# Kernel tuning notes

Hardware: AMD Instinct MI355X
Metric: run time of the kernel (lower is better)

Reference implementation:

```python
import jax, jax.numpy as jnp
import numpy as np

K = 16          # k_neighbours
BIG = 1e9       # distance penalty for masked senders


def setup_inputs() -> dict:
    key = jax.random.key(0)
    ks = jax.random.split(key, 8)
    B, N, F, H, FO = 64, 512, 64, 128, 64
    nodes = jax.random.normal(ks[0], (B, N, F), jnp.float32)
    mask = jax.random.randint(ks[1], (B, N), 0, 2, jnp.int32)

    def w(k_, sh):
        return jax.random.normal(k_, sh, jnp.float32) * (1.0 / np.sqrt(sh[0]).astype(np.float32))

    We1 = w(ks[2], (2 * F, H)); be1 = jnp.zeros((H,), jnp.float32)
    We2 = w(ks[3], (H, H));     be2 = jnp.zeros((H,), jnp.float32)
    Wn1 = w(ks[4], (F + H, H)); bn1 = jnp.zeros((H,), jnp.float32)
    Wn2 = w(ks[5], (H, FO));    bn2 = jnp.zeros((FO,), jnp.float32)
    return dict(nodes=nodes, mask=mask, We1=We1, be1=be1, We2=We2, be2=be2,
                Wn1=Wn1, bn1=bn1, Wn2=Wn2, bn2=bn2)


def reference(nodes, mask, We1, be1, We2, be2, Wn1, bn1, Wn2, bn2):
    # nodes: [B,N,F] ; mask: [B,N] (1 = real node, 0 = padding)
    m = mask.astype(nodes.dtype)                      # [B,N]
    x = nodes * m[..., None]                          # zero padded nodes

    # --- dynamic kNN graph (euclidean_squared + top_k, no self connection) ---
    sq = jnp.sum(x * x, axis=-1)                      # [B,N]
    dist = jnp.abs(sq[:, :, None] + sq[:, None, :]
                   - 2.0 * jnp.einsum('bnf,bmf->bnm', x, x))  # [B,N,N]
    dist = dist + BIG * (1.0 - m)[:, None, :]         # never select masked senders
    _, idx = jax.lax.top_k(-dist, K + 1)              # [B,N,K+1]
    idx = idx[..., 1:]                                # drop self connection -> [B,N,K]

    # --- gather sender features / masks along edges ---
    gathered = jax.vmap(lambda xf, ib: xf[ib])(x, idx)    # [B,N,K,F]
    smask = jax.vmap(lambda mv, ib: mv[ib])(m, idx)       # [B,N,K]
    recv = jnp.broadcast_to(x[:, :, None, :], gathered.shape)
    edges = jnp.concatenate([recv, gathered], axis=-1)    # [B,N,K,2F] ('concat' aggregation)

    # --- edge MLP (gather-compute) ---
    h = jax.nn.relu(edges @ We1 + be1)
    h = jax.nn.relu(h @ We2 + be2)                        # [B,N,K,H]

    # --- masked mean pooling over edges (scatter back to nodes) ---
    emask = m[:, :, None] * smask                         # edge valid iff both endpoints valid
    h = h * emask[..., None]
    cnt = jnp.maximum(jnp.sum(emask, axis=-1, keepdims=True), 1.0)  # [B,N,1]
    pooled = jnp.sum(h, axis=2) / cnt                     # [B,N,H]

    # --- node update MLP ---
    nh = jnp.concatenate([x, pooled], axis=-1)            # [B,N,F+H]
    out = jax.nn.relu(nh @ Wn1 + bn1) @ Wn2 + bn2         # [B,N,FO]
    return out * m[..., None]                             # zero padded nodes in output
```

## Files before the change

### kernel.cpp

```cpp
#include <hip/hip_runtime.h>

#define DI __device__ __forceinline__

typedef __bf16 bf16_t;
typedef __bf16 bf16x4 __attribute__((ext_vector_type(4)));
typedef __bf16 bf16x8 __attribute__((ext_vector_type(8)));
typedef float f32x4 __attribute__((ext_vector_type(4)));
typedef unsigned long long u64;


DI bf16_t f2b(float f) {
  unsigned u = __float_as_uint(f);
  unsigned r = (u + 0x7fffu + ((u >> 16) & 1u)) >> 16;
  return __builtin_bit_cast(bf16_t, (unsigned short)r);
}
DI float b2f(bf16_t h) {
  return __uint_as_float(((unsigned)__builtin_bit_cast(unsigned short, h)) << 16);
}
DI f32x4 zero4() { f32x4 z = {0.f, 0.f, 0.f, 0.f}; return z; }

DI bf16x8 make_frag(const float* p, bool wantlo) {
  float4 v0 = *(const float4*)p;
  float4 v1 = *(const float4*)(p + 4);
  float vv[8] = {v0.x, v0.y, v0.z, v0.w, v1.x, v1.y, v1.z, v1.w};
  bf16x8 a;
#pragma unroll
  for (int j = 0; j < 8; ++j) {
    bf16_t hi = f2b(vv[j]);
    a[j] = wantlo ? f2b(vv[j] - b2f(hi)) : hi;
  }
  return a;
}

DI u64 u64min(u64 a, u64 b) { return a < b ? a : b; }
template <int CTRL>
DI u64 dpp_u64(u64 v) {
  int lo = (int)(unsigned)(v & 0xffffffffull);
  int hi = (int)(unsigned)(v >> 32);
  int tlo = __builtin_amdgcn_update_dpp(0, lo, CTRL, 0xF, 0xF, true);
  int thi = __builtin_amdgcn_update_dpp(0, hi, CTRL, 0xF, 0xF, true);
  return (((u64)(unsigned)thi) << 32) | (unsigned)tlo;
}
template <int CTRL>
DI float dpp_f32(float v) {
  int t = __builtin_amdgcn_update_dpp(0, (int)__float_as_uint(v), CTRL, 0xF, 0xF, true);
  return __uint_as_float((unsigned)t);
}
DI u64 rowmin_u64(u64 v) {
  v = u64min(v, dpp_u64<0xB1>(v));
  v = u64min(v, dpp_u64<0x4E>(v));
  v = u64min(v, dpp_u64<0x141>(v));
  v = u64min(v, dpp_u64<0x140>(v));
  return v;
}
DI float rowsum_f32(float v) {
  v += dpp_f32<0xB1>(v);
  v += dpp_f32<0x4E>(v);
  v += dpp_f32<0x141>(v);
  v += dpp_f32<0x140>(v);
  return v;
}
DI void bitonic16(u64* a) {
#pragma unroll
  for (int k = 2; k <= 16; k <<= 1)
#pragma unroll
    for (int j = k >> 1; j > 0; j >>= 1)
#pragma unroll
      for (int i = 0; i < 16; ++i) {
        const int l = i ^ j;
        if (l > i) {
          const bool up = ((i & k) == 0);
          const bool sw = up ? (a[i] > a[l]) : (a[i] < a[l]);
          const u64 t0 = a[i], t1 = a[l];
          a[i] = sw ? t1 : t0;
          a[l] = sw ? t0 : t1;
        }
      }
}

__global__ void __launch_bounds__(256) kfuse(const float* __restrict__ nodes,
    const int* __restrict__ mask,
    const float* __restrict__ We1, const float* __restrict__ We2,
    const float* __restrict__ Wn1, const float* __restrict__ Wn2,
    float* __restrict__ x, bf16_t* __restrict__ xhi, bf16_t* __restrict__ xlo,
    float* __restrict__ sq, int* __restrict__ vlist, int* __restrict__ vcnt,
    bf16_t* __restrict__ W1p, bf16_t* __restrict__ W2p,
    bf16_t* __restrict__ Wn1p, bf16_t* __restrict__ Wn2p) {
  const int blk = blockIdx.x, t = threadIdx.x;
  __shared__ int cnts[8];
  __shared__ int basep[8];

  if (blk < 512) {
    const int b = blk >> 3, n0 = (blk & 7) * 64;
#pragma unroll
    for (int i = 0; i < 4; ++i) {
      const int idx = t + 256 * i;
      const int gi = b * 512 + n0 + (idx >> 4);
      const int fo = (idx & 15) * 4;
      const float fm = (float)mask[gi];
      const size_t ro = (size_t)gi * 64;
      float4 v = *(const float4*)(nodes + ro + fo);
      v.x *= fm; v.y *= fm; v.z *= fm; v.w *= fm;
      *(float4*)(x + ro + fo) = v;
      float vv[4] = {v.x, v.y, v.z, v.w};
      bf16x4 hh, ll;
#pragma unroll
      for (int k = 0; k < 4; ++k) {
        bf16_t hi = f2b(vv[k]);
        hh[k] = hi;
        ll[k] = f2b(vv[k] - b2f(hi));
      }
      *(bf16x4*)(xhi + ro + fo) = hh;
      *(bf16x4*)(xlo + ro + fo) = ll;
      float s = v.x * v.x + v.y * v.y + v.z * v.z + v.w * v.w;
      s = rowsum_f32(s);
      if ((t & 15) == 0) sq[gi] = s;
    }
  } else if (blk < 576) {
    const int b = blk - 512, lane = t & 63, w = t >> 6;
    unsigned long long bal[2]; int flag[2];
#pragma unroll
    for (int h = 0; h < 2; ++h) {
      flag[h] = (mask[b * 512 + h * 256 + t] != 0);
      bal[h] = __ballot(flag[h]);
      if (lane == 0) cnts[h * 4 + w] = __popcll(bal[h]);
    }
    __syncthreads();
    if (t == 0) {
      int a = 0;
      for (int c = 0; c < 8; ++c) { basep[c] = a; a += cnts[c]; }
      vcnt[b] = a;
    }
    __syncthreads();
#pragma unroll
    for (int h = 0; h < 2; ++h) {
      if (flag[h]) {
        const unsigned long long lt = (lane == 0) ? 0ull : (~0ull >> (64 - lane));
        const int pos = basep[h * 4 + w] + __popcll(bal[h] & lt);
        vlist[b * 512 + pos] = h * 256 + t;
      }
    }
  } else {
    int p = (blk - 576) * 256 + t;
    const float* W; bf16_t* dst; int K, Nn, local, mode;
    if (p < 4096)       { W = We1; dst = W1p;  K = 128; Nn = 128; mode = 0; local = p; }
    else if (p < 8192)  { W = We2; dst = W2p;  K = 128; Nn = 128; mode = 1; local = p - 4096; }
    else if (p < 14336) { W = Wn1; dst = Wn1p; K = 192; Nn = 128; mode = 0; local = p - 8192; }
    else                { W = Wn2; dst = Wn2p; K = 128; Nn = 64;  mode = 1; local = p - 14336; }
    int lane = local & 63;
    int nnt = (Nn >> 4);
    int chunk = local >> 6;
    int nt = chunk % nnt;
    int s = chunk / nnt;
    int n = nt * 16 + (lane & 15);
    int kbase = s * 32 + ((lane >> 4) * 8);
    bf16x8 v;
#pragma unroll
    for (int j = 0; j < 8; ++j) {
      int kp = kbase + j;
      int region = kp / K;
      int kk = kp - region * K;
      float w = W[kk * Nn + n];
      bf16_t hi = f2b(w);
      v[j] = (mode == 1 && region == 1) ? f2b(w - b2f(hi)) : hi;
    }
    *(bf16x8*)(dst + (size_t)local * 8) = v;
  }
}

__global__ void __launch_bounds__(256) kknn(const float* __restrict__ x,
    const float* __restrict__ sq, const int* __restrict__ vlist,
    const int* __restrict__ vcnt, int* __restrict__ idxg) {
  const int b = blockIdx.x & 63, tile = blockIdx.x >> 6;
  const int nv = vcnt[b];
  if (tile * 16 >= nv) return;
  const int t = threadIdx.x, lane = t & 63, w = t >> 6;
  const int i = lane >> 4, d = lane & 15;
  __shared__ float sqs[512];
  __shared__ int vls[512];
  __shared__ __align__(16) float xr[16 * 64];
  __shared__ __align__(16) float xc[64 * 68];
  for (int k = t; k < 512; k += 256) { sqs[k] = sq[b * 512 + k]; vls[k] = vlist[b * 512 + k]; }
  __syncthreads();
  const float* xb = x + (size_t)b * 512 * 64;
  {
    const int r = t >> 4, f4 = (t & 15) * 4;
    const int slot = tile * 16 + r;
    const int row = vls[slot < nv ? slot : 0];
    *(float4*)(xr + r * 64 + f4) = *(const float4*)(xb + (size_t)row * 64 + f4);
  }
  const int rslot = tile * 16 + w * 4 + i;
  const bool vrow = (rslot < nv);
  const int nrow = vls[rslot < nv ? rslot : 0];
  const float sqn = sqs[nrow];
  __syncthreads();
  const float4 xn = *(const float4*)(xr + (w * 4 + i) * 64 + d * 4);

  float dotv[32];
#pragma unroll
  for (int j = 0; j < 32; ++j) dotv[j] = 0.f;

#pragma unroll
  for (int cb = 0; cb < 8; ++cb) {
    if (cb * 64 < nv) {
      __syncthreads();
      {
        const int fo = (t & 15) * 4;
#pragma unroll
        for (int p = 0; p < 4; ++p) {
          const int cl = (t >> 4) + p * 16;
          const int c = cb * 64 + cl;
          if (c < nv)
            *(float4*)(xc + cl * 68 + fo) = *(const float4*)(xb + (size_t)vls[c] * 64 + fo);
        }
      }
      __syncthreads();
#pragma unroll
      for (int q = 0; q < 4; ++q) {
        float dq = 0.f;
#pragma unroll 4
        for (int cc = 0; cc < 16; ++cc) {
          const float4 xm = *(const float4*)(xc + (q * 16 + cc) * 68 + d * 4);
          float p = xn.x * xm.x;
          p = fmaf(xn.y, xm.y, p);
          p = fmaf(xn.z, xm.z, p);
          p = fmaf(xn.w, xm.w, p);
          p = rowsum_f32(p);
          dq = (d == cc) ? p : dq;
        }
        dotv[cb * 4 + q] = dq;
      }
    }
  }

  const u64 INF64 = ~0ull;
  u64 s1[16], s2[16];
#pragma unroll
  for (int j = 0; j < 16; ++j) { s1[j] = INF64; s2[j] = INF64; }
#pragma unroll
  for (int j = 0; j < 32; ++j) {
    if (j * 16 < nv) {
      const int c = j * 16 + d;
      const int m = vls[c < nv ? c : 0];
      const float dd = fabsf(sqn + sqs[m] - 2.f * dotv[j]);
      const u64 key = (((u64)__float_as_uint(dd)) << 32) | (unsigned)m;
      const bool ok = (c < nv) && (m != nrow);
      if (j < 16) s1[j] = ok ? key : INF64;
      else        s2[j - 16] = ok ? key : INF64;
    }
  }
  bitonic16(s1);
  const bool two = (nv > 256);
  if (two) bitonic16(s2);

  int res = nrow;
#pragma unroll
  for (int ts = 0; ts < 16; ++ts) {
    const u64 head = two ? u64min(s1[0], s2[0]) : s1[0];
    const u64 wmin = rowmin_u64(head);
    if (d == ts) res = (wmin == INF64) ? nrow : (int)(unsigned)(wmin & 0xffffffffull);
    const bool w1 = (wmin != INF64) && (s1[0] == wmin);
#pragma unroll
    for (int k = 0; k < 15; ++k) s1[k] = w1 ? s1[k + 1] : s1[k];
    s1[15] = w1 ? INF64 : s1[15];
    if (two) {
      const bool w2 = (wmin != INF64) && (s2[0] == wmin);
#pragma unroll
      for (int k = 0; k < 15; ++k) s2[k] = w2 ? s2[k + 1] : s2[k];
      s2[15] = w2 ? INF64 : s2[15];
    }
  }
  if (vrow) idxg[((size_t)b * 512 + rslot) * 16 + d] = res;
}

__global__ void __launch_bounds__(256, 2) kedge(const bf16_t* __restrict__ xhi,
    const bf16_t* __restrict__ xlo, const int* __restrict__ idxg,
    const int* __restrict__ vlist, const int* __restrict__ vcnt,
    const bf16_t* __restrict__ W1p, const bf16_t* __restrict__ W2p,
    const float* __restrict__ be1, const float* __restrict__ be2,
    float* __restrict__ pooled) {
  __shared__ __align__(16) bf16_t wbuf[32768];
  __shared__ __align__(16) bf16_t hfrag[4][2][1024];
  const int t = threadIdx.x, lane = t & 63, w = t >> 6;
  const int q = lane >> 4, e = lane & 15;
  const int bb = blockIdx.x & 63;
  const int s0 = ((blockIdx.x >> 6) * 4 + w) * 2;

  {
    const uint4* s1 = (const uint4*)W1p;
    const uint4* s2 = (const uint4*)W2p;
    uint4* dst = (uint4*)wbuf;
#pragma unroll
    for (int i = 0; i < 8; ++i) dst[t + 256 * i] = s1[t + 256 * i];
#pragma unroll
    for (int i = 0; i < 8; ++i) dst[2048 + t + 256 * i] = s2[t + 256 * i];
  }
  __syncthreads();

  const int nv = vcnt[bb];
  if (s0 >= nv) return;

  int vl[2], sv[2];
  {
#pragma unroll
    for (int u = 0; u < 2; ++u) {
      const int sl = (s0 + u) < nv ? (s0 + u) : 0;
      vl[u] = vlist[bb * 512 + sl];
      sv[u] = idxg[((size_t)(bb * 512 + sl) << 4) + e];
    }
  }

  for (int base = s0; base < nv; base += 64) {
    const bool act1 = (base + 1) < nv;
    const int gid0 = bb * 512 + vl[0];
    const int gid1 = bb * 512 + vl[1];
    const size_t rb0 = (size_t)gid0 << 6;
    const size_t rb1 = (size_t)gid1 << 6;
    const size_t nb0 = (size_t)(bb * 512 + sv[0]) << 6;
    const size_t nb1 = (size_t)(bb * 512 + sv[1]) << 6;

    bf16x8 af[2][8];
#pragma unroll
    for (int k = 0; k < 4; ++k) {
      const int off = (k & 1) * 32 + q * 8;
      const bf16_t* pl = (k >> 1) ? xlo : xhi;
      af[0][k]     = *(const bf16x8*)(pl + rb0 + off);
      af[1][k]     = *(const bf16x8*)(pl + rb1 + off);
      af[0][4 + k] = *(const bf16x8*)(pl + nb0 + off);
      af[1][4 + k] = *(const bf16x8*)(pl + nb1 + off);
    }

    int nvl[2] = {vl[0], vl[1]}, nsv[2] = {sv[0], sv[1]};
    {
      const int nb = base + 64;
      if (nb < nv) {
#pragma unroll
        for (int u = 0; u < 2; ++u) {
          const int sl = (nb + u) < nv ? (nb + u) : 0;
          nvl[u] = vlist[bb * 512 + sl];
          nsv[u] = idxg[((size_t)(bb * 512 + sl) << 4) + e];
        }
      }
    }

    f32x4 acc[2][8];
#pragma unroll
    for (int u = 0; u < 2; ++u)
#pragma unroll
      for (int nt = 0; nt < 8; ++nt) acc[u][nt] = zero4();

#pragma unroll
    for (int ph = 0; ph < 2; ++ph)
#pragma unroll
      for (int k = 0; k < 4; ++k) {
        const bf16_t* wb = wbuf + (ph * 2 + (k & 1)) * 4096;
        const bf16x8 a0 = af[0][ph * 4 + k];
        const bf16x8 a1 = af[1][ph * 4 + k];
#pragma unroll
        for (int nt = 0; nt < 8; ++nt) {
          const bf16x8 bfv = *(const bf16x8*)(wb + (nt * 64 + lane) * 8);
          acc[0][nt] = __builtin_amdgcn_mfma_f32_16x16x32_bf16(a0, bfv, acc[0][nt], 0, 0, 0);
          acc[1][nt] = __builtin_amdgcn_mfma_f32_16x16x32_bf16(a1, bfv, acc[1][nt], 0, 0, 0);
        }
      }

    f32x4 acc2[2][8];
#pragma unroll
    for (int u = 0; u < 2; ++u)
#pragma unroll
      for (int nt = 0; nt < 8; ++nt) acc2[u][nt] = zero4();

#pragma unroll
    for (int hh = 0; hh < 2; ++hh) {
#pragma unroll
      for (int u = 0; u < 2; ++u)
#pragma unroll
        for (int nt4 = 0; nt4 < 4; ++nt4) {
          const int nt = hh * 4 + nt4;
          const int cc = nt * 16 + e;
          const float bv = be1[cc];
          const int bse = (((cc >> 5) & 1) * 64 + q * 4 + 16 * ((cc >> 3) & 3)) * 8 + (cc & 7);
#pragma unroll
          for (int r = 0; r < 4; ++r)
            hfrag[w][u][bse + r * 8] = f2b(fmaxf(acc[u][nt][r] + bv, 0.f));
        }
#pragma unroll
      for (int sl = 0; sl < 2; ++sl) {
        const int f = hh * 2 + sl;
        const bf16x8 a20 = *(const bf16x8*)(&hfrag[w][0][(sl * 64 + lane) * 8]);
        const bf16x8 a21 = *(const bf16x8*)(&hfrag[w][1][(sl * 64 + lane) * 8]);
        const bf16_t* wb2 = wbuf + 16384 + f * 4096;
#pragma unroll
        for (int nt = 0; nt < 8; ++nt) {
          const bf16x8 bfv = *(const bf16x8*)(wb2 + (nt * 64 + lane) * 8);
          acc2[0][nt] = __builtin_amdgcn_mfma_f32_16x16x32_bf16(a20, bfv, acc2[0][nt], 0, 0, 0);
          acc2[1][nt] = __builtin_amdgcn_mfma_f32_16x16x32_bf16(a21, bfv, acc2[1][nt], 0, 0, 0);
        }
      }
    }

#pragma unroll
    for (int u = 0; u < 2; ++u) {
      if (u == 0 || act1) {
        const int gid = u ? gid1 : gid0;
#pragma unroll
        for (int nt = 0; nt < 8; ++nt) {
          const float bv = be2[nt * 16 + e];
          float part = 0.f;
#pragma unroll
          for (int r = 0; r < 4; ++r) part += fmaxf(acc2[u][nt][r] + bv, 0.f);
          part += __shfl_xor(part, 16, 64);
          part += __shfl_xor(part, 32, 64);
          if (lane < 16) pooled[(size_t)gid * 128 + nt * 16 + lane] = part * 0.0625f;
        }
      }
    }

    vl[0] = nvl[0]; vl[1] = nvl[1];
    sv[0] = nsv[0]; sv[1] = nsv[1];
  }
}

__global__ void __launch_bounds__(256) knode(const float* __restrict__ x,
    const float* __restrict__ pooled, const int* __restrict__ mask,
    const bf16_t* __restrict__ Wn1p, const bf16_t* __restrict__ Wn2p,
    const float* __restrict__ bn1, const float* __restrict__ bn2,
    float* __restrict__ out) {
  __shared__ __align__(16) bf16_t wbuf[8192];
  __shared__ __align__(16) bf16_t hfrag[4][2][2048];
  const int t = threadIdx.x, lane = t & 63, w = t >> 6;
  const int q = lane >> 4, e = lane & 15;
  int nodebase[2];
#pragma unroll
  for (int u = 0; u < 2; ++u) nodebase[u] = (blockIdx.x * 8 + w * 2 + u) * 16;

  f32x4 acc[2][8];
#pragma unroll
  for (int u = 0; u < 2; ++u)
#pragma unroll
    for (int nt = 0; nt < 8; ++nt) acc[u][nt] = zero4();

#pragma unroll
  for (int ph = 0; ph < 3; ++ph) {
    __syncthreads();
    {
      const uint4* src = (const uint4*)(Wn1p + (size_t)ph * 8192);
      uint4* dst = (uint4*)wbuf;
#pragma unroll
      for (int i = 0; i < 4; ++i) dst[t + 256 * i] = src[t + 256 * i];
    }
    __syncthreads();
#pragma unroll
    for (int k = 0; k < 4; ++k) {
      const int s = 2 * ph + (k & 1) + (k >> 1) * 6;
      const bool wantlo = (s >= 6);
      const int sr = wantlo ? (s - 6) : s;
      const int col = sr * 32 + q * 8;
      bf16x8 af[2];
#pragma unroll
      for (int u = 0; u < 2; ++u) {
        const int node = nodebase[u] + e;
        const float* p = (col < 64) ? (x + (size_t)node * 64 + col)
                                    : (pooled + (size_t)node * 128 + (col - 64));
        af[u] = make_frag(p, wantlo);
      }
      const int bslab = s & 1;
#pragma unroll
      for (int nt = 0; nt < 8; ++nt) {
        const bf16x8 bfv = *(const bf16x8*)(wbuf + bslab * 4096 + (nt * 64 + lane) * 8);
#pragma unroll
        for (int u = 0; u < 2; ++u)
          acc[u][nt] = __builtin_amdgcn_mfma_f32_16x16x32_bf16(af[u], bfv, acc[u][nt], 0, 0, 0);
      }
    }
  }

#pragma unroll
  for (int u = 0; u < 2; ++u) {
#pragma unroll
    for (int nt = 0; nt < 8; ++nt) {
      const int cc = nt * 16 + e;
      const float bv = bn1[cc];
      const int base = ((cc >> 5) * 64 + (q * 4) + 16 * ((cc >> 3) & 3)) * 8 + (cc & 7);
#pragma unroll
      for (int r = 0; r < 4; ++r) {
        float h = fmaxf(acc[u][nt][r] + bv, 0.f);
        hfrag[w][u][base + r * 8] = f2b(h);
      }
    }
  }

  f32x4 acc2[2][4];
#pragma unroll
  for (int u = 0; u < 2; ++u)
#pragma unroll
    for (int nt = 0; nt < 4; ++nt) acc2[u][nt] = zero4();

  __syncthreads();
  {
    const uint4* src = (const uint4*)Wn2p;
    uint4* dst = (uint4*)wbuf;
#pragma unroll
    for (int i = 0; i < 4; ++i) dst[t + 256 * i] = src[t + 256 * i];
  }
  __syncthreads();
#pragma unroll
  for (int sl = 0; sl < 4; ++sl) {
    bf16x8 af[2];
#pragma unroll
    for (int u = 0; u < 2; ++u)
      af[u] = *(const bf16x8*)(&hfrag[w][u][(sl * 64 + lane) * 8]);
#pragma unroll
    for (int nt = 0; nt < 4; ++nt) {
      const bf16x8 bfv = *(const bf16x8*)(wbuf + sl * 2048 + (nt * 64 + lane) * 8);
#pragma unroll
      for (int u = 0; u < 2; ++u)
        acc2[u][nt] = __builtin_amdgcn_mfma_f32_16x16x32_bf16(af[u], bfv, acc2[u][nt], 0, 0, 0);
    }
  }

#pragma unroll
  for (int u = 0; u < 2; ++u) {
    int mm[4];
#pragma unroll
    for (int r = 0; r < 4; ++r) mm[r] = mask[nodebase[u] + q * 4 + r];
#pragma unroll
    for (int nt = 0; nt < 4; ++nt) {
      const float bv = bn2[nt * 16 + e];
#pragma unroll
      for (int r = 0; r < 4; ++r) {
        const int node = nodebase[u] + q * 4 + r;
        out[(size_t)node * 64 + nt * 16 + e] = (acc2[u][nt][r] + bv) * (float)mm[r];
      }
    }
  }
}

extern "C" void kernel_launch(void* const* d_in, const int* in_sizes, int n_in,
                              void* d_out, int out_size, void* d_ws, size_t ws_size,
                              hipStream_t stream) {
  const float* nodes = (const float*)d_in[0];
  const int*   mask  = (const int*)d_in[1];
  const float* We1   = (const float*)d_in[2];
  const float* be1   = (const float*)d_in[3];
  const float* We2   = (const float*)d_in[4];
  const float* be2   = (const float*)d_in[5];
  const float* Wn1   = (const float*)d_in[6];
  const float* bn1   = (const float*)d_in[7];
  const float* Wn2   = (const float*)d_in[8];
  const float* bn2   = (const float*)d_in[9];
  float* out = (float*)d_out;

  char* p = (char*)d_ws;
  auto alloc = [&](size_t bytes) -> char* {
    char* r = p;
    p += (bytes + 255) & ~(size_t)255;
    return r;
  };
  float*  x      = (float*)alloc((size_t)32768 * 64 * 4);
  bf16_t* xhi    = (bf16_t*)alloc((size_t)32768 * 64 * 2);
  bf16_t* xlo    = (bf16_t*)alloc((size_t)32768 * 64 * 2);
  float*  sq     = (float*)alloc((size_t)32768 * 4);
  int*    vlist  = (int*)alloc((size_t)32768 * 4);
  int*    vcnt   = (int*)alloc((size_t)64 * 4);
  int*    idxg   = (int*)alloc((size_t)32768 * 16 * 4);
  float*  pooled = (float*)alloc((size_t)32768 * 128 * 4);
  bf16_t* W1p    = (bf16_t*)alloc((size_t)8 * 8 * 64 * 8 * 2);
  bf16_t* W2p    = (bf16_t*)alloc((size_t)8 * 8 * 64 * 8 * 2);
  bf16_t* Wn1p   = (bf16_t*)alloc((size_t)12 * 8 * 64 * 8 * 2);
  bf16_t* Wn2p   = (bf16_t*)alloc((size_t)8 * 4 * 64 * 8 * 2);
  if ((size_t)(p - (char*)d_ws) > ws_size) return;

  kfuse<<<640, 256, 0, stream>>>(nodes, mask, We1, We2, Wn1, Wn2,
                                 x, xhi, xlo, sq, vlist, vcnt, W1p, W2p, Wn1p, Wn2p);
  kknn<<<2048, 256, 0, stream>>>(x, sq, vlist, vcnt, idxg);
  kedge<<<512, 256, 0, stream>>>(xhi, xlo, idxg, vlist, vcnt, W1p, W2p, be1, be2, pooled);
  knode<<<256, 256, 0, stream>>>(x, pooled, mask, Wn1p, Wn2p, bn1, bn2, out);
}
```

Before: 189.2 us.

## Compute kNN dot products with split-bf16 MFMA instead of scalar FP32 shuffles

Replaces the FP32 per-lane dot-product loop with cross-lane row reductions in the kNN kernel by 16x16x32 bf16 MFMA tiles. The hi and lo bf16 parts are combined with four MFMAs per K-chunk to approximate FP32 accuracy. Candidate rows are loaded straight from global memory into registers, with the next tile prefetched, instead of being staged through shared memory. The dot matrix is written to shared memory for the top-k stage. This is meant to remove the shuffle-heavy ALU work and the repeated syncthreads, at the cost of a small precision change that could alter near-tie neighbour choices.

```diff
diff --git a/kernel.cpp b/kernel.cpp
--- a/kernel.cpp
+++ b/kernel.cpp
@@ -168,7 +168,8 @@
   }
 }
 
-__global__ void __launch_bounds__(256) kknn(const float* __restrict__ x,
+__global__ void __launch_bounds__(256) kknn(const bf16_t* __restrict__ xhi,
+    const bf16_t* __restrict__ xlo,
     const float* __restrict__ sq, const int* __restrict__ vlist,
     const int* __restrict__ vcnt, int* __restrict__ idxg) {
   const int b = blockIdx.x & 63, tile = blockIdx.x >> 6;
@@ -178,60 +179,69 @@
   const int i = lane >> 4, d = lane & 15;
   __shared__ float sqs[512];
   __shared__ int vls[512];
-  __shared__ __align__(16) float xr[16 * 64];
-  __shared__ __align__(16) float xc[64 * 68];
+  __shared__ __align__(16) float S[16 * 520];
   for (int k = t; k < 512; k += 256) { sqs[k] = sq[b * 512 + k]; vls[k] = vlist[b * 512 + k]; }
   __syncthreads();
-  const float* xb = x + (size_t)b * 512 * 64;
-  {
-    const int r = t >> 4, f4 = (t & 15) * 4;
-    const int slot = tile * 16 + r;
-    const int row = vls[slot < nv ? slot : 0];
-    *(float4*)(xr + r * 64 + f4) = *(const float4*)(xb + (size_t)row * 64 + f4);
-  }
+
+  const size_t xb = (size_t)b * 512 * 64;
+
+  const int aslot = tile * 16 + d;
+  const int arow = vls[aslot < nv ? aslot : 0];
+  bf16x8 ah[2], al[2];
+#pragma unroll
+  for (int kh = 0; kh < 2; ++kh) {
+    ah[kh] = *(const bf16x8*)(xhi + xb + (size_t)arow * 64 + kh * 32 + i * 8);
+    al[kh] = *(const bf16x8*)(xlo + xb + (size_t)arow * 64 + kh * 32 + i * 8);
+  }
+
   const int rslot = tile * 16 + w * 4 + i;
   const bool vrow = (rslot < nv);
   const int nrow = vls[rslot < nv ? rslot : 0];
   const float sqn = sqs[nrow];
+
+  int crs[8];
+#pragma unroll
+  for (int jj = 0; jj < 8; ++jj) {
+    const int c = (w + 4 * jj) * 16 + d;
+    crs[jj] = vls[c < nv ? c : 0];
+  }
+
+  bf16x8 bh[2], bl[2];
+  if (w * 16 < nv) {
+#pragma unroll
+    for (int kh = 0; kh < 2; ++kh) {
+      bh[kh] = *(const bf16x8*)(xhi + xb + (size_t)crs[0] * 64 + kh * 32 + i * 8);
+      bl[kh] = *(const bf16x8*)(xlo + xb + (size_t)crs[0] * 64 + kh * 32 + i * 8);
+    }
+  }
+  for (int jj = 0; jj < 8; ++jj) {
+    const int ct = w + 4 * jj;
+    if (ct * 16 >= nv) break;
+    bf16x8 nbh[2], nbl[2];
+    const bool pre = (jj < 7) && ((w + 4 * (jj + 1)) * 16 < nv);
+    if (pre) {
+#pragma unroll
+      for (int kh = 0; kh < 2; ++kh) {
+        nbh[kh] = *(const bf16x8*)(xhi + xb + (size_t)crs[jj + 1] * 64 + kh * 32 + i * 8);
+        nbl[kh] = *(const bf16x8*)(xlo + xb + (size_t)crs[jj + 1] * 64 + kh * 32 + i * 8);
+      }
+    }
+    f32x4 acc = zero4();
+#pragma unroll
+    for (int kh = 0; kh < 2; ++kh) {
+      acc = __builtin_amdgcn_mfma_f32_16x16x32_bf16(ah[kh], bh[kh], acc, 0, 0, 0);
+      acc = __builtin_amdgcn_mfma_f32_16x16x32_bf16(ah[kh], bl[kh], acc, 0, 0, 0);
+      acc = __builtin_amdgcn_mfma_f32_16x16x32_bf16(al[kh], bh[kh], acc, 0, 0, 0);
+      acc = __builtin_amdgcn_mfma_f32_16x16x32_bf16(al[kh], bl[kh], acc, 0, 0, 0);
+    }
+#pragma unroll
+    for (int r = 0; r < 4; ++r) S[(i * 4 + r) * 520 + ct * 16 + d] = acc[r];
+    if (pre) {
+#pragma unroll
+      for (int kh = 0; kh < 2; ++kh) { bh[kh] = nbh[kh]; bl[kh] = nbl[kh]; }
+    }
+  }
   __syncthreads();
-  const float4 xn = *(const float4*)(xr + (w * 4 + i) * 64 + d * 4);
-
-  float dotv[32];
-#pragma unroll
-  for (int j = 0; j < 32; ++j) dotv[j] = 0.f;
-
-#pragma unroll
-  for (int cb = 0; cb < 8; ++cb) {
-    if (cb * 64 < nv) {
-      __syncthreads();
-      {
-        const int fo = (t & 15) * 4;
-#pragma unroll
-        for (int p = 0; p < 4; ++p) {
-          const int cl = (t >> 4) + p * 16;
-          const int c = cb * 64 + cl;
-          if (c < nv)
-            *(float4*)(xc + cl * 68 + fo) = *(const float4*)(xb + (size_t)vls[c] * 64 + fo);
-        }
-      }
-      __syncthreads();
-#pragma unroll
-      for (int q = 0; q < 4; ++q) {
-        float dq = 0.f;
-#pragma unroll 4
-        for (int cc = 0; cc < 16; ++cc) {
-          const float4 xm = *(const float4*)(xc + (q * 16 + cc) * 68 + d * 4);
-          float p = xn.x * xm.x;
-          p = fmaf(xn.y, xm.y, p);
-          p = fmaf(xn.z, xm.z, p);
-          p = fmaf(xn.w, xm.w, p);
-          p = rowsum_f32(p);
-          dq = (d == cc) ? p : dq;
-        }
-        dotv[cb * 4 + q] = dq;
-      }
-    }
-  }
 
   const u64 INF64 = ~0ull;
   u64 s1[16], s2[16];
@@ -242,7 +252,8 @@
     if (j * 16 < nv) {
       const int c = j * 16 + d;
       const int m = vls[c < nv ? c : 0];
-      const float dd = fabsf(sqn + sqs[m] - 2.f * dotv[j]);
+      const float dot = S[(w * 4 + i) * 520 + j * 16 + d];
+      const float dd = fabsf(sqn + sqs[m] - 2.f * dot);
       const u64 key = (((u64)__float_as_uint(dd)) << 32) | (unsigned)m;
       const bool ok = (c < nv) && (m != nrow);
       if (j < 16) s1[j] = ok ? key : INF64;
@@ -573,7 +584,7 @@
 
   kfuse<<<640, 256, 0, stream>>>(nodes, mask, We1, We2, Wn1, Wn2,
                                  x, xhi, xlo, sq, vlist, vcnt, W1p, W2p, Wn1p, Wn2p);
-  kknn<<<2048, 256, 0, stream>>>(x, sq, vlist, vcnt, idxg);
+  kknn<<<2048, 256, 0, stream>>>(xhi, xlo, sq, vlist, vcnt, idxg);
   kedge<<<512, 256, 0, stream>>>(xhi, xlo, idxg, vlist, vcnt, W1p, W2p, be1, be2, pooled);
   knode<<<256, 256, 0, stream>>>(x, pooled, mask, Wn1p, Wn2p, bn1, bn2, out);
 }
```

Result: faster. 166.6 us (-12.0%).
